# Performance work log

Hardware: AMD Instinct MI355X
Metric: run time of the kernel (lower is better)

The kernel has to match this reference:

```python
import jax, jax.numpy as jnp
import numpy as np

NUM_GROUPS = 8
EPS = 1e-5


def group_norm(x, gamma, beta):
    # x: [B, C, H, W], groups over channel dim
    b, c, h, w = x.shape
    xg = x.reshape(b, NUM_GROUPS, c // NUM_GROUPS, h, w)
    mean = xg.mean(axis=(2, 3, 4), keepdims=True)
    var = xg.var(axis=(2, 3, 4), keepdims=True)
    xg = (xg - mean) * jax.lax.rsqrt(var + EPS)
    x = xg.reshape(b, c, h, w)
    return x * gamma[None, :, None, None] + beta[None, :, None, None]


def conv1x1(x, w, bias):
    # 1x1 conv == per-pixel linear: [B,C,H,W] x [O,C] -> [B,O,H,W]
    return jnp.einsum('bchw,oc->bohw', x, w) + bias[None, :, None, None]


def setup_inputs() -> dict:
    key = jax.random.key(0)
    ks = jax.random.split(key, 6)
    B, C, H, W = 16, 512, 32, 32
    s = 1.0 / np.sqrt(C)  # conv2d default init scale-ish
    return {
        'x': jax.random.normal(ks[0], (B, C, H, W), jnp.float32),
        'gn_w': jnp.ones((C,), jnp.float32),
        'gn_b': jnp.zeros((C,), jnp.float32),
        'wq': jax.random.normal(ks[1], (C, C), jnp.float32) * s,
        'bq': jnp.zeros((C,), jnp.float32),
        'wk': jax.random.normal(ks[2], (C, C), jnp.float32) * s,
        'bk': jnp.zeros((C,), jnp.float32),
        'wv': jax.random.normal(ks[3], (C, C), jnp.float32) * s,
        'bv': jnp.zeros((C,), jnp.float32),
        'wo': jax.random.normal(ks[4], (C, C), jnp.float32) * s,
        'bo': jnp.zeros((C,), jnp.float32),
    }


def reference(x, gn_w, gn_b, wq, bq, wk, bk, wv, bv, wo, bo):
    b, c, h, w = x.shape
    scale = c ** (-0.5)
    hn = group_norm(x, gn_w, gn_b)
    q = conv1x1(hn, wq, bq).reshape(b, c, h * w).transpose(0, 2, 1)  # [B, N, C]
    k = conv1x1(hn, wk, bk).reshape(b, c, h * w).transpose(0, 2, 1)  # [B, N, C]
    v = conv1x1(hn, wv, bv).reshape(b, c, h * w).transpose(0, 2, 1)  # [B, N, C]
    attn = jnp.einsum('bnc,bmc->bnm', q, k) * scale                 # [B, N, N]
    attn = jax.nn.softmax(attn, axis=-1)
    out = jnp.einsum('bnm,bmc->bnc', attn, v)                       # [B, N, C]
    out = out.transpose(0, 2, 1).reshape(b, c, h, w)
    out = conv1x1(out, wo, bo)
    return x + out
```

## Files before the change

kernel.cpp:

```cpp
#include <hip/hip_runtime.h>
#include <stdint.h>

#define C_DIM 512
#define HW_N  1024
#define CPG   64
#define EPS_GN 1e-5f
#define SCALE_QK 0.044194173824159216f

typedef __attribute__((ext_vector_type(8))) __bf16 bf16x8v;
typedef __attribute__((ext_vector_type(4))) float  f32x4;

typedef __attribute__((address_space(1))) void gvoid_t;
typedef __attribute__((address_space(3))) void lvoid_t;

__device__ __forceinline__ void gload_lds16(const void* g, void* l) {
  __builtin_amdgcn_global_load_lds((gvoid_t*)g, (lvoid_t*)l, 16, 0, 0);
}

__device__ __forceinline__ uint16_t f2bfbits(float f) {
  __bf16 h = (__bf16)f;
  return __builtin_bit_cast(uint16_t, h);
}

__device__ __forceinline__ float bf2f(uint16_t u) {
  return __builtin_bit_cast(float, (uint32_t)u << 16);
}

template<int N>
__device__ __forceinline__ void vm_wait() {
  if constexpr (N == 0)      asm volatile("s_waitcnt vmcnt(0)" ::: "memory");
  else if constexpr (N == 3) asm volatile("s_waitcnt vmcnt(3)" ::: "memory");
  else if constexpr (N == 4) asm volatile("s_waitcnt vmcnt(4)" ::: "memory");
  else if constexpr (N == 6) asm volatile("s_waitcnt vmcnt(6)" ::: "memory");
}

__global__ __launch_bounds__(256)
void gn_stats(const float* __restrict__ x, float2* __restrict__ part)
{
  const int lin  = blockIdx.x;
  const int b    = lin >> 4;
  const int g    = (lin >> 1) & 7;
  const int half = lin & 1;
  const int t    = threadIdx.x;

  const float4* xv = (const float4*)(x + ((long long)(b * C_DIM + g * CPG)) * HW_N
                                       + half * 512);
  float s1 = 0.f, s2 = 0.f;
  for (int i = t; i < 64 * 128; i += 256) {
    const int c  = i >> 7;
    const int nf = i & 127;
    float4 v = xv[c * 256 + nf];
    s1 += v.x + v.y + v.z + v.w;
    s2 += v.x * v.x + v.y * v.y + v.z * v.z + v.w * v.w;
  }
  #pragma unroll
  for (int off = 32; off; off >>= 1) {
    s1 += __shfl_xor(s1, off);
    s2 += __shfl_xor(s2, off);
  }
  __shared__ float red[2][4];
  const int w = t >> 6, l = t & 63;
  if (l == 0) { red[0][w] = s1; red[1][w] = s2; }
  __syncthreads();
  if (t == 0) {
    s1 = red[0][0] + red[0][1] + red[0][2] + red[0][3];
    s2 = red[1][0] + red[1][1] + red[1][2] + red[1][3];
    part[lin] = make_float2(s1, s2);
  }
}

__global__ __launch_bounds__(512)
void gn_norm(const float* __restrict__ x, const float2* __restrict__ part,
             const float* __restrict__ gnw, const float* __restrict__ gnb,
             __bf16* __restrict__ hn)
{
  const int b  = blockIdx.x >> 4;
  const int nc = blockIdx.x & 15;
  const int t  = threadIdx.x;

  __shared__ float asc[512], bsc[512];
  __shared__ float tile[64][65];

  {
    const int c = t;
    const int g = c >> 6;
    float2 p0 = part[(b * 8 + g) * 2 + 0];
    float2 p1 = part[(b * 8 + g) * 2 + 1];
    const float mean = (p0.x + p1.x) * (1.f / 65536.f);
    const float var  = (p0.y + p1.y) * (1.f / 65536.f) - mean * mean;
    const float rstd = rsqrtf(var + EPS_GN);
    const float a = rstd * gnw[c];
    asc[c] = a;
    bsc[c] = gnb[c] - mean * a;
  }
  __syncthreads();

  const long long xb = (long long)b * C_DIM * HW_N + nc * 64;
  __bf16* ob = hn + ((long long)b * HW_N + nc * 64) * C_DIM;

  for (int cg = 0; cg < 8; ++cg) {
    #pragma unroll
    for (int pass = 0; pass < 2; ++pass) {
      const int task = pass * 512 + t;
      const int c  = task >> 4;
      const int f4 = task & 15;
      float4 v = *(const float4*)(x + xb + (long long)(cg * 64 + c) * HW_N + f4 * 4);
      const float a  = asc[cg * 64 + c];
      const float bb = bsc[cg * 64 + c];
      tile[c][f4 * 4 + 0] = v.x * a + bb;
      tile[c][f4 * 4 + 1] = v.y * a + bb;
      tile[c][f4 * 4 + 2] = v.z * a + bb;
      tile[c][f4 * 4 + 3] = v.w * a + bb;
    }
    __syncthreads();
    {
      const int n  = t >> 3;
      const int gc = t & 7;
      uint32_t p[4];
      #pragma unroll
      for (int j = 0; j < 4; ++j) {
        const float f0 = tile[gc * 8 + 2 * j + 0][n];
        const float f1 = tile[gc * 8 + 2 * j + 1][n];
        p[j] = (uint32_t)f2bfbits(f0) | ((uint32_t)f2bfbits(f1) << 16);
      }
      *(uint4*)(ob + (long long)n * C_DIM + cg * 64 + gc * 8) =
          make_uint4(p[0], p[1], p[2], p[3]);
    }
    __syncthreads();
  }
}

__global__ __launch_bounds__(256)
void prep_kernel(const float* __restrict__ wq, const float* __restrict__ wk,
                 const float* __restrict__ wv, const float* __restrict__ wo,
                 const float* __restrict__ bq, const float* __restrict__ bk,
                 __bf16* __restrict__ wqkb, __bf16* __restrict__ wvb,
                 __bf16* __restrict__ wob, float* __restrict__ bqk)
{
  const int blk = blockIdx.x;
  if (blk < 1024) {
    const int which = blk >> 8;
    const int i = (blk & 255) * 256 + threadIdx.x;
    const float* src = (which == 0) ? wq : (which == 1) ? wk : (which == 2) ? wv : wo;
    __bf16* dst = (which == 0) ? wqkb
               : (which == 1) ? (wqkb + (size_t)C_DIM * C_DIM)
               : (which == 2) ? wvb : wob;
    const float scale = (which == 0) ? SCALE_QK : 1.f;
    float4 v = ((const float4*)src)[i];
    uint32_t lo = (uint32_t)f2bfbits(v.x * scale) | ((uint32_t)f2bfbits(v.y * scale) << 16);
    uint32_t hi = (uint32_t)f2bfbits(v.z * scale) | ((uint32_t)f2bfbits(v.w * scale) << 16);
    ((uint2*)dst)[i] = make_uint2(lo, hi);
  } else {
    for (int j = threadIdx.x; j < 1024; j += 256)
      bqk[j] = (j < 512) ? bq[j] * SCALE_QK : bk[j - 512];
  }
}

__global__ __launch_bounds__(256)
void softmax_kernel(__bf16* __restrict__ S)
{
  const long long row = blockIdx.x;
  uint2* sp = (uint2*)(S + row * HW_N);
  const int t = threadIdx.x;
  uint2 raw = sp[t];
  float v0 = bf2f((uint16_t)(raw.x & 0xffff));
  float v1 = bf2f((uint16_t)(raw.x >> 16));
  float v2 = bf2f((uint16_t)(raw.y & 0xffff));
  float v3 = bf2f((uint16_t)(raw.y >> 16));
  float m = fmaxf(fmaxf(v0, v1), fmaxf(v2, v3));
  #pragma unroll
  for (int off = 32; off; off >>= 1) m = fmaxf(m, __shfl_xor(m, off));
  __shared__ float redm[4];
  __shared__ float reds[4];
  const int w = t >> 6, l = t & 63;
  if (l == 0) redm[w] = m;
  __syncthreads();
  m = fmaxf(fmaxf(redm[0], redm[1]), fmaxf(redm[2], redm[3]));
  float e0 = __expf(v0 - m), e1 = __expf(v1 - m);
  float e2 = __expf(v2 - m), e3 = __expf(v3 - m);
  float sum = e0 + e1 + e2 + e3;
  #pragma unroll
  for (int off = 32; off; off >>= 1) sum += __shfl_xor(sum, off);
  if (l == 0) reds[w] = sum;
  __syncthreads();
  sum = reds[0] + reds[1] + reds[2] + reds[3];
  const float inv = 1.f / sum;
  uint32_t lo = (uint32_t)f2bfbits(e0 * inv) | ((uint32_t)f2bfbits(e1 * inv) << 16);
  uint32_t hi = (uint32_t)f2bfbits(e2 * inv) | ((uint32_t)f2bfbits(e3 * inv) << 16);
  sp[t] = make_uint2(lo, hi);
}

#define QMFMA(QA, QB, BREG)                                                    \
  do {                                                                         \
    __builtin_amdgcn_s_setprio(1);                                             \
    _Pragma("unroll")                                                          \
    for (int f_ = 0; f_ < 4; ++f_)                                             \
      _Pragma("unroll")                                                        \
      for (int c_ = 0; c_ < 2; ++c_)                                           \
        _Pragma("unroll")                                                      \
        for (int kk_ = 0; kk_ < 2; ++kk_)                                      \
          acc[QA][QB][f_][c_] = __builtin_amdgcn_mfma_f32_16x16x32_bf16(       \
              Ar[f_][kk_], BREG[c_][kk_], acc[QA][QB][f_][c_], 0, 0, 0);       \
    __builtin_amdgcn_s_setprio(0);                                             \
  } while (0)

#define LGKM0_FENCE()                                                          \
  asm volatile("s_waitcnt lgkmcnt(0)" ::: "memory");                           \
  __builtin_amdgcn_sched_barrier(0)

template<int BIASM>
__global__ __launch_bounds__(512, 2)
void gemm256(const __bf16* __restrict__ Amat, const __bf16* __restrict__ Bmat,
             __bf16* __restrict__ Cmat, const float* __restrict__ bias,
             int lda, int ldb, int ldc,
             long long aS, long long bS, long long cS, int K)
{
  __shared__ alignas(16) char lds[131072];

  const int tt = threadIdx.x;
  const int w  = tt >> 6;
  const int l  = tt & 63;
  const int lr = l & 15;
  const int lg = l >> 4;
  const int wm = w >> 2;
  const int wn = w & 3;
  const int b  = blockIdx.z;
  const int n0 = blockIdx.x * 256;
  const int m0 = blockIdx.y * 256;

  const __bf16* Ab = Amat + (long long)b * aS;
  const __bf16* Bb = Bmat + (long long)b * bS;

  const int r0  = tt >> 3;
  const int sg8 = ((tt & 7) ^ ((tt >> 3) & 7)) << 3;

  f32x4 acc[2][2][4][2];
  #pragma unroll
  for (int qa = 0; qa < 2; ++qa)
    #pragma unroll
    for (int qb = 0; qb < 2; ++qb)
      #pragma unroll
      for (int f = 0; f < 4; ++f)
        #pragma unroll
        for (int c = 0; c < 2; ++c)
          acc[qa][qb][f][c] = (f32x4){0.f, 0.f, 0.f, 0.f};

  auto stage = [&](int kt, int h) {
    char* dst = lds + ((kt & 1) << 16) + (h << 14) + w * 1024;
    const long long ld = (h < 2) ? lda : ldb;
    const __bf16* src = ((h < 2) ? Ab + (long long)(m0 + (h & 1) * 128) * lda
                                 : Bb + (long long)(n0 + (h & 1) * 128) * ldb)
                        + (long long)kt * 64 + sg8;
    gload_lds16(src + (long long)r0 * ld, dst);
    gload_lds16(src + (long long)(r0 + 64) * ld, dst + 8192);
  };
  auto rdA = [&](const char* bb, int qa, int f, int kk) -> bf16x8v {
    const int r = wm * 64 + f * 16 + lr;
    return *(const bf16x8v*)(bb + (qa << 14) + r * 128
                             + (((kk * 4 + lg) ^ (r & 7)) << 4));
  };
  auto rdB = [&](const char* bb, int qb, int c, int kk) -> bf16x8v {
    const int r = wn * 32 + c * 16 + lr;
    return *(const bf16x8v*)(bb + 32768 + (qb << 14) + r * 128
                             + (((kk * 4 + lg) ^ (r & 7)) << 4));
  };

  const int NT = K >> 6;

  stage(0, 0); stage(0, 1); stage(0, 2); stage(0, 3);
  stage(1, 0); stage(1, 2); stage(1, 3);
  vm_wait<6>();
  __builtin_amdgcn_s_barrier();

  bf16x8v Ar[4][2], B0r[2][2], B1r[2][2];

  for (int t = 0; t < NT; ++t) {
    const char* buf = lds + ((t & 1) << 16);

    #pragma unroll
    for (int f = 0; f < 4; ++f)
      #pragma unroll
      for (int kk = 0; kk < 2; ++kk) Ar[f][kk] = rdA(buf, 0, f, kk);
    #pragma unroll
    for (int c = 0; c < 2; ++c)
      #pragma unroll
      for (int kk = 0; kk < 2; ++kk) B0r[c][kk] = rdB(buf, 0, c, kk);
    if (t + 1 < NT) stage(t + 1, 1);
    __builtin_amdgcn_s_barrier();
    LGKM0_FENCE();
    QMFMA(0, 0, B0r);
    __builtin_amdgcn_s_barrier();
    __builtin_amdgcn_sched_barrier(0);

    #pragma unroll
    for (int c = 0; c < 2; ++c)
      #pragma unroll
      for (int kk = 0; kk < 2; ++kk) B1r[c][kk] = rdB(buf, 1, c, kk);
    if (t + 2 < NT) stage(t + 2, 0);
    __builtin_amdgcn_s_barrier();
    LGKM0_FENCE();
    QMFMA(0, 1, B1r);
    __builtin_amdgcn_s_barrier();
    __builtin_amdgcn_sched_barrier(0);

    #pragma unroll
    for (int f = 0; f < 4; ++f)
      #pragma unroll
      for (int kk = 0; kk < 2; ++kk) Ar[f][kk] = rdA(buf, 1, f, kk);
    if (t + 2 < NT) stage(t + 2, 2);
    __builtin_amdgcn_s_barrier();
    LGKM0_FENCE();
    QMFMA(1, 1, B1r);
    __builtin_amdgcn_s_barrier();
    __builtin_amdgcn_sched_barrier(0);

    if (t + 2 < NT) stage(t + 2, 3);
    QMFMA(1, 0, B0r);
    if (t + 2 < NT) vm_wait<6>();
    else            vm_wait<0>();
    __builtin_amdgcn_s_barrier();
    __builtin_amdgcn_sched_barrier(0);
  }

  __bf16* Cb = Cmat + (long long)b * cS;
  #pragma unroll
  for (int qa = 0; qa < 2; ++qa) {
    #pragma unroll
    for (int f = 0; f < 4; ++f) {
      const int rrb = m0 + qa * 128 + wm * 64 + f * 16 + lg * 4;
      #pragma unroll
      for (int qb = 0; qb < 2; ++qb) {
        #pragma unroll
        for (int c = 0; c < 2; ++c) {
          const int cc = n0 + qb * 128 + wn * 32 + c * 16 + lr;
          const float cbias = (BIASM == 1) ? bias[cc] : 0.f;
          #pragma unroll
          for (int r = 0; r < 4; ++r) {
            const int rr = rrb + r;
            float v = acc[qa][qb][f][c][r];
            if (BIASM == 1) v += cbias;
            if (BIASM == 2) v += bias[rr];
            Cb[(long long)rr * ldc + cc] = (__bf16)v;
          }
        }
      }
    }
  }
}

template<int BM, int OUTM, int BIASM>
__global__ __launch_bounds__(512, 2)
void gemm8(const __bf16* __restrict__ Amat, const __bf16* __restrict__ Bmat,
           void* __restrict__ Cmat,
           const float* __restrict__ bias,
           const float* __restrict__ resid,
           int lda, int ldb, int ldc,
           long long aS, long long bS, long long cS, int K)
{
  constexpr int TILE_B = BM * 64 + 16384;
  constexpr int CA = BM / 128;
  constexpr int CH = CA + 2;
  constexpr int FPR = BM / 32;
  constexpr int FPP = FPR / 2;

  __shared__ alignas(16) char lds[3 * TILE_B];

  const int tt = threadIdx.x;
  const int w  = tt >> 6;
  const int l  = tt & 63;
  const int lr = l & 15;
  const int lg = l >> 4;
  const int wm = w >> 2;
  const int wn = w & 3;
  const int b  = blockIdx.z;
  const int n0 = blockIdx.x * 256;
  const int m0 = blockIdx.y * BM;

  const __bf16* Ab = Amat + (long long)b * aS;
  const __bf16* Bb = Bmat + (long long)b * bS;

  const int srow = tt >> 2;
  const int sgr  = (tt & 3) ^ ((tt >> 3) & 3);

  f32x4 acc[FPR][4];
  #pragma unroll
  for (int f = 0; f < FPR; ++f)
    #pragma unroll
    for (int c = 0; c < 4; ++c)
      acc[f][c] = (f32x4){0.f, 0.f, 0.f, 0.f};

  auto stage = [&](int t, int c) {
    const int k0 = t << 5;
    char* dst = lds + (t % 3) * TILE_B + c * 8192 + w * 1024;
    const __bf16* src;
    if (c < CA) src = Ab + (long long)(m0 + c * 128 + srow) * lda + k0 + sgr * 8;
    else        src = Bb + (long long)(n0 + (c - CA) * 128 + srow) * ldb + k0 + sgr * 8;
    gload_lds16(src, dst);
  };
  auto rdA = [&](const char* base, int f) -> bf16x8v {
    const int row = wm * (BM / 2) + f * 16 + lr;
    return *(const bf16x8v*)(base + row * 64 + ((lg ^ ((row >> 1) & 3)) << 4));
  };
  auto rdB = [&](const char* base, int c) -> bf16x8v {
    const int row = wn * 64 + c * 16 + lr;
    return *(const bf16x8v*)(base + BM * 64 + row * 64 + ((lg ^ ((row >> 1) & 3)) << 4));
  };

  const int NT = K >> 5;

  #pragma unroll
  for (int c = 0; c < CH; ++c) stage(0, c);
  #pragma unroll
  for (int c = 0; c < CH; ++c) stage(1, c);

  for (int t = 0; t < NT; ++t) {
    const char* buf = lds + (t % 3) * TILE_B;
    if (t + 1 < NT) vm_wait<CH>();
    else            vm_wait<0>();
    __builtin_amdgcn_s_barrier();
    __builtin_amdgcn_sched_barrier(0);

    bf16x8v Bf[4];
    #pragma unroll
    for (int c = 0; c < 4; ++c) Bf[c] = rdB(buf, c);
    bf16x8v Af[FPP];
    #pragma unroll
    for (int f = 0; f < FPP; ++f) Af[f] = rdA(buf, f);
    if (t + 2 < NT) { stage(t + 2, 0); stage(t + 2, 1); }
    LGKM0_FENCE();
    __builtin_amdgcn_s_setprio(1);
    #pragma unroll
    for (int f = 0; f < FPP; ++f)
      #pragma unroll
      for (int c = 0; c < 4; ++c)
        acc[f][c] = __builtin_amdgcn_mfma_f32_16x16x32_bf16(Af[f], Bf[c], acc[f][c], 0, 0, 0);
    __builtin_amdgcn_s_setprio(0);
    __builtin_amdgcn_s_barrier();
    __builtin_amdgcn_sched_barrier(0);

    bf16x8v Ag[FPP];
    #pragma unroll
    for (int f = 0; f < FPP; ++f) Ag[f] = rdA(buf, FPP + f);
    if (t + 2 < NT) {
      #pragma unroll
      for (int c = 2; c < CH; ++c) stage(t + 2, c);
    }
    LGKM0_FENCE();
    __builtin_amdgcn_s_setprio(1);
    #pragma unroll
    for (int f = 0; f < FPP; ++f)
      #pragma unroll
      for (int c = 0; c < 4; ++c)
        acc[FPP + f][c] = __builtin_amdgcn_mfma_f32_16x16x32_bf16(Ag[f], Bf[c], acc[FPP + f][c], 0, 0, 0);
    __builtin_amdgcn_s_setprio(0);
    __builtin_amdgcn_s_barrier();
    __builtin_amdgcn_sched_barrier(0);
  }

  #pragma unroll
  for (int f = 0; f < FPR; ++f) {
    const int rrb = m0 + wm * (BM / 2) + f * 16 + lg * 4;
    #pragma unroll
    for (int c = 0; c < 4; ++c) {
      const int cc = n0 + wn * 64 + c * 16 + lr;
      const float cbias = (BIASM == 1) ? bias[cc] : 0.f;
      #pragma unroll
      for (int r = 0; r < 4; ++r) {
        const int rr = rrb + r;
        float v = acc[f][c][r];
        if (BIASM == 1) v += cbias;
        if (BIASM == 2) v += bias[rr];
        const long long idx = (long long)rr * ldc + cc;
        if (OUTM == 0) {
          ((__bf16*)Cmat + (long long)b * cS)[idx] = (__bf16)v;
        } else if (OUTM == 2) {
          ((float*)Cmat + (long long)b * cS)[idx] = v;
        } else {
          float* Cf = (float*)Cmat + (long long)b * cS;
          const float* Rf = resid + (long long)b * cS;
          Cf[idx] = v + Rf[idx];
        }
      }
    }
  }
}

extern "C" void kernel_launch(void* const* d_in, const int* in_sizes, int n_in,
                              void* d_out, int out_size, void* d_ws, size_t ws_size,
                              hipStream_t stream)
{
  const float* x   = (const float*)d_in[0];
  const float* gnw = (const float*)d_in[1];
  const float* gnb = (const float*)d_in[2];
  const float* wq  = (const float*)d_in[3];
  const float* bq  = (const float*)d_in[4];
  const float* wk  = (const float*)d_in[5];
  const float* bk  = (const float*)d_in[6];
  const float* wv  = (const float*)d_in[7];
  const float* bv  = (const float*)d_in[8];
  const float* wo  = (const float*)d_in[9];
  const float* bo  = (const float*)d_in[10];
  (void)in_sizes; (void)n_in; (void)out_size; (void)ws_size;

  size_t used = 0;
  char* base = (char*)d_ws;
  auto carve = [&](size_t bytes) -> void* {
    used = (used + 255) & ~(size_t)255;
    void* p = base + used;
    used += bytes;
    return p;
  };

  __bf16* wqkb = (__bf16*)carve((size_t)2 * C_DIM * C_DIM * 2);
  __bf16* wvb  = (__bf16*)carve((size_t)C_DIM * C_DIM * 2);
  __bf16* wob  = (__bf16*)carve((size_t)C_DIM * C_DIM * 2);
  float*  bqk  = (float*) carve((size_t)1024 * 4);
  float2* part = (float2*)carve((size_t)256 * 8);

  __bf16* hn   = (__bf16*)carve((size_t)16 * HW_N * C_DIM * 2);
  __bf16* qkb  = (__bf16*)carve((size_t)16 * HW_N * 1024 * 2);
  __bf16* vtb  = (__bf16*)carve((size_t)16 * C_DIM * HW_N * 2);
  __bf16* o1b  = (__bf16*)carve((size_t)16 * HW_N * C_DIM * 2);
  __bf16* Sb   = (__bf16*)carve((size_t)16 * HW_N * HW_N * 2);

  const long long sNC = (long long)HW_N * C_DIM;
  const long long sNN = (long long)HW_N * 1024;

  prep_kernel<<<dim3(1025), 256, 0, stream>>>(wq, wk, wv, wo, bq, bk,
                                              wqkb, wvb, wob, bqk);
  gn_stats<<<dim3(256), 256, 0, stream>>>(x, part);
  gn_norm<<<dim3(256), 512, 0, stream>>>(x, part, gnw, gnb, hn);

  gemm256<1><<<dim3(4, 4, 16), 512, 0, stream>>>(hn, wqkb, qkb, bqk,
      C_DIM, C_DIM, 1024, sNC, 0, sNN, C_DIM);

  gemm256<2><<<dim3(4, 2, 16), 512, 0, stream>>>(wvb, hn, vtb, bv,
      C_DIM, C_DIM, HW_N, 0, sNC, sNC, C_DIM);

  gemm256<0><<<dim3(4, 4, 16), 512, 0, stream>>>(qkb, qkb + 512, Sb, nullptr,
      1024, 1024, 1024, sNN, sNN, sNN, C_DIM);

  softmax_kernel<<<dim3(16 * 1024), 256, 0, stream>>>(Sb);

  gemm256<0><<<dim3(2, 4, 16), 512, 0, stream>>>(Sb, vtb, o1b, nullptr,
      1024, 1024, C_DIM, sNN, sNC, sNC, HW_N);

  gemm8<128, 1, 2><<<dim3(4, 4, 16), 512, 0, stream>>>(wob, o1b, (float*)d_out, bo, x,
      C_DIM, C_DIM, HW_N, 0, sNC, sNC, C_DIM);
}
```

Measured before the change: 168.7 us.

## Remap GEMM blocks per XCD and retile V and PV GEMMs to 128-row tiles

Adds an XCD-aware block-index decode so that consecutive logical tiles (same batch) land on the same XCD, improving L2 reuse across the chiplets. All GEMMs now launch flat 1D grids of 256 blocks. The V projection and attention-times-V GEMMs switch from 256x256 tiles to the 128-row gemm8 kernel, which raises the block count so the 256 CUs are better filled. The cost is extra integer divides per block and smaller tiles with less reuse for the retiled GEMMs.

```diff
diff --git a/kernel.cpp b/kernel.cpp
--- a/kernel.cpp
+++ b/kernel.cpp
@@ -32,6 +32,19 @@
   else if constexpr (N == 3) asm volatile("s_waitcnt vmcnt(3)" ::: "memory");
   else if constexpr (N == 4) asm volatile("s_waitcnt vmcnt(4)" ::: "memory");
   else if constexpr (N == 6) asm volatile("s_waitcnt vmcnt(6)" ::: "memory");
+}
+
+struct BlkId { int bx, by, bz; };
+__device__ __forceinline__ BlkId xcd_decode(int gx, int gy) {
+  const int nwg = gridDim.x;
+  const int bid = blockIdx.x;
+  const int wg  = (bid & 7) * (nwg >> 3) + (bid >> 3);
+  const int pb  = gx * gy;
+  const int bz  = wg / pb;
+  const int rem = wg - bz * pb;
+  const int by  = rem / gx;
+  const int bx  = rem - by * gx;
+  return {bx, by, bz};
 }
 
 __global__ __launch_bounds__(256)
@@ -213,7 +226,7 @@
 void gemm256(const __bf16* __restrict__ Amat, const __bf16* __restrict__ Bmat,
              __bf16* __restrict__ Cmat, const float* __restrict__ bias,
              int lda, int ldb, int ldc,
-             long long aS, long long bS, long long cS, int K)
+             long long aS, long long bS, long long cS, int K, int gx, int gy)
 {
   __shared__ alignas(16) char lds[131072];
 
@@ -224,9 +237,10 @@
   const int lg = l >> 4;
   const int wm = w >> 2;
   const int wn = w & 3;
-  const int b  = blockIdx.z;
-  const int n0 = blockIdx.x * 256;
-  const int m0 = blockIdx.y * 256;
+  const BlkId bk_ = xcd_decode(gx, gy);
+  const int b  = bk_.bz;
+  const int n0 = bk_.bx * 256;
+  const int m0 = bk_.by * 256;
 
   const __bf16* Ab = Amat + (long long)b * aS;
   const __bf16* Bb = Bmat + (long long)b * bS;
@@ -355,7 +369,7 @@
            const float* __restrict__ bias,
            const float* __restrict__ resid,
            int lda, int ldb, int ldc,
-           long long aS, long long bS, long long cS, int K)
+           long long aS, long long bS, long long cS, int K, int gx, int gy)
 {
   constexpr int TILE_B = BM * 64 + 16384;
   constexpr int CA = BM / 128;
@@ -372,9 +386,10 @@
   const int lg = l >> 4;
   const int wm = w >> 2;
   const int wn = w & 3;
-  const int b  = blockIdx.z;
-  const int n0 = blockIdx.x * 256;
-  const int m0 = blockIdx.y * BM;
+  const BlkId bk_ = xcd_decode(gx, gy);
+  const int b  = bk_.bz;
+  const int n0 = bk_.bx * 256;
+  const int m0 = bk_.by * BM;
 
   const __bf16* Ab = Amat + (long long)b * aS;
   const __bf16* Bb = Bmat + (long long)b * bS;
@@ -531,20 +546,20 @@
   gn_stats<<<dim3(256), 256, 0, stream>>>(x, part);
   gn_norm<<<dim3(256), 512, 0, stream>>>(x, part, gnw, gnb, hn);
 
-  gemm256<1><<<dim3(4, 4, 16), 512, 0, stream>>>(hn, wqkb, qkb, bqk,
-      C_DIM, C_DIM, 1024, sNC, 0, sNN, C_DIM);
-
-  gemm256<2><<<dim3(4, 2, 16), 512, 0, stream>>>(wvb, hn, vtb, bv,
-      C_DIM, C_DIM, HW_N, 0, sNC, sNC, C_DIM);
-
-  gemm256<0><<<dim3(4, 4, 16), 512, 0, stream>>>(qkb, qkb + 512, Sb, nullptr,
-      1024, 1024, 1024, sNN, sNN, sNN, C_DIM);
+  gemm256<1><<<dim3(256), 512, 0, stream>>>(hn, wqkb, qkb, bqk,
+      C_DIM, C_DIM, 1024, sNC, 0, sNN, C_DIM, 4, 4);
+
+  gemm8<128, 0, 2><<<dim3(256), 512, 0, stream>>>(wvb, hn, vtb, bv, nullptr,
+      C_DIM, C_DIM, HW_N, 0, sNC, sNC, C_DIM, 4, 4);
+
+  gemm256<0><<<dim3(256), 512, 0, stream>>>(qkb, qkb + 512, Sb, nullptr,
+      1024, 1024, 1024, sNN, sNN, sNN, C_DIM, 4, 4);
 
   softmax_kernel<<<dim3(16 * 1024), 256, 0, stream>>>(Sb);
 
-  gemm256<0><<<dim3(2, 4, 16), 512, 0, stream>>>(Sb, vtb, o1b, nullptr,
-      1024, 1024, C_DIM, sNN, sNC, sNC, HW_N);
-
-  gemm8<128, 1, 2><<<dim3(4, 4, 16), 512, 0, stream>>>(wob, o1b, (float*)d_out, bo, x,
-      C_DIM, C_DIM, HW_N, 0, sNC, sNC, C_DIM);
-}
+  gemm8<128, 0, 0><<<dim3(256), 512, 0, stream>>>(Sb, vtb, o1b, nullptr, nullptr,
+      1024, 1024, C_DIM, sNN, sNC, sNC, HW_N, 2, 8);
+
+  gemm8<128, 1, 2><<<dim3(256), 512, 0, stream>>>(wob, o1b, (float*)d_out, bo, x,
+      C_DIM, C_DIM, HW_N, 0, sNC, sNC, C_DIM, 4, 4);
+}
```

Result: faster. 149.7 us (-11.3%).
